# Optimization experiments

Measured on AMD Instinct MI355X. Metric: run time of the kernel, lower is better.

Reference implementation:

```python
import jax, jax.numpy as jnp
import numpy as np

R = 16
ALPHA = 16.0
SCALING = ALPHA / R  # = 1.0


def setup_inputs() -> dict:
    key = jax.random.key(0)
    k1, k2, k3 = jax.random.split(key, 3)
    x = jax.random.normal(k1, (4, 4096, 4096), dtype=jnp.float32)
    A = jax.random.normal(k2, (4096, R), dtype=jnp.float32)
    B = jax.random.normal(k3, (R, 4096), dtype=jnp.float32)
    return {"x": x, "A": A, "B": B}


def reference(x, A, B):
    # Faithful to torch: W_delta = A @ B * scaling; out = x @ W_delta
    # (dropout_p=0.0 so dropout is a no-op)
    W_delta = (A @ B) * SCALING  # [in, out]
    return jnp.matmul(x, W_delta)  # [b, s, out]
```

## Files before the change

kernel.cpp:

```cpp
#include <hip/hip_runtime.h>

constexpr int RANK = 16;
constexpr int K = 4096;
constexpr int N = 4096;
constexpr int M = 4 * 4096;
constexpr int KC = 512;
constexpr int NCHUNK = K / KC;

__global__ __launch_bounds__(256) void lora_fused(const float* __restrict__ x,
                                                  const float* __restrict__ A,
                                                  const float* __restrict__ B,
                                                  float* __restrict__ out) {
  const int lane = threadIdx.x & 63;
  const int tid = threadIdx.x;
  const int wave = tid >> 6;
  const int rbase = blockIdx.x * 16;
  const int r0 = rbase + wave * 4;

  __shared__ float4 As[KC * 4];
  __shared__ float Ts[16][RANK];

  const float4* __restrict__ A4 = reinterpret_cast<const float4*>(A);

  float vals[64];
#pragma unroll
  for (int i = 0; i < 64; ++i) vals[i] = 0.0f;

  for (int c = 0; c < NCHUNK; ++c) {
    __syncthreads();
#pragma unroll
    for (int q = 0; q < 8; ++q) {
      const int n = q * 256 + tid;
      const int k = n >> 2;
      const int s = n & 3;
      const int p = s ^ ((k >> 2) & 3);
      As[k * 4 + p] = A4[(size_t)c * 2048 + n];
    }
    __syncthreads();

    const int m = (lane >> 2) & 3;
#pragma unroll
    for (int kbi = 0; kbi < 8; ++kbi) {
      const int kl = kbi * 64 + lane;
      const size_t kg = (size_t)c * KC + kl;

      float xv[4];
#pragma unroll
      for (int r = 0; r < 4; ++r) xv[r] = x[(size_t)(r0 + r) * K + kg];

      float4 a[4];
#pragma unroll
      for (int s = 0; s < 4; ++s) a[s] = As[kl * 4 + (s ^ m)];

#pragma unroll
      for (int r = 0; r < 4; ++r) {
#pragma unroll
        for (int s = 0; s < 4; ++s) {
          vals[r * 16 + 4 * s + 0] = fmaf(xv[r], a[s].x, vals[r * 16 + 4 * s + 0]);
          vals[r * 16 + 4 * s + 1] = fmaf(xv[r], a[s].y, vals[r * 16 + 4 * s + 1]);
          vals[r * 16 + 4 * s + 2] = fmaf(xv[r], a[s].z, vals[r * 16 + 4 * s + 2]);
          vals[r * 16 + 4 * s + 3] = fmaf(xv[r], a[s].w, vals[r * 16 + 4 * s + 3]);
        }
      }
    }
  }

#define RSTEP(HALF)                                            \
  {                                                            \
    const bool hi = (lane & (HALF)) != 0;                      \
    _Pragma("unroll")                                          \
    for (int i = 0; i < (HALF); ++i) {                         \
      const float send = hi ? vals[i] : vals[i + (HALF)];      \
      const float keep = hi ? vals[i + (HALF)] : vals[i];      \
      vals[i] = keep + __shfl_xor(send, (HALF), 64);           \
    }                                                          \
  }
  RSTEP(32)
  RSTEP(16)
  RSTEP(8)
  RSTEP(4)
  RSTEP(2)
  RSTEP(1)
#undef RSTEP

  Ts[wave * 4 + (lane >> 4)][lane & 15] = vals[0];
  __syncthreads();

  const int n0 = wave * 1024 + lane * 4;
  const float4* __restrict__ B4 = reinterpret_cast<const float4*>(B);
  float4* __restrict__ out4 = reinterpret_cast<float4*>(out);

#pragma unroll 1
  for (int cc = 0; cc < 4; ++cc) {
    const int col = wave * 1024 + cc * 256 + lane * 4;

    float4 b[16];
#pragma unroll
    for (int j = 0; j < RANK; ++j) b[j] = B4[((size_t)j * N + col) >> 2];

#pragma unroll 1
    for (int r = 0; r < 16; ++r) {
      const float4* __restrict__ tr4 =
          reinterpret_cast<const float4*>(&Ts[r][0]);
      const float4 t0 = tr4[0];
      const float4 t1 = tr4[1];
      const float4 t2 = tr4[2];
      const float4 t3 = tr4[3];

      float4 acc;
      acc.x = acc.y = acc.z = acc.w = 0.0f;
      const float tsv[16] = {t0.x, t0.y, t0.z, t0.w, t1.x, t1.y, t1.z, t1.w,
                             t2.x, t2.y, t2.z, t2.w, t3.x, t3.y, t3.z, t3.w};
#pragma unroll
      for (int j = 0; j < RANK; ++j) {
        acc.x = fmaf(tsv[j], b[j].x, acc.x);
        acc.y = fmaf(tsv[j], b[j].y, acc.y);
        acc.z = fmaf(tsv[j], b[j].z, acc.z);
        acc.w = fmaf(tsv[j], b[j].w, acc.w);
      }
      out4[((size_t)(rbase + r) * N + col) >> 2] = acc;
    }
  }
  (void)n0;
}

extern "C" void kernel_launch(void* const* d_in, const int* in_sizes, int n_in,
                              void* d_out, int out_size, void* d_ws, size_t ws_size,
                              hipStream_t stream) {
  const float* x = (const float*)d_in[0];
  const float* A = (const float*)d_in[1];
  const float* B = (const float*)d_in[2];
  float* out = (float*)d_out;
  (void)d_ws; (void)ws_size;

  lora_fused<<<M / 16, 256, 0, stream>>>(x, A, B, out);
}
```

Baseline: 129.7 us.

## Double-buffer A chunks in LDS using direct global-to-LDS async loads

Replaces the register-staged copy of A into shared memory with __builtin_amdgcn_global_load_lds into a two-slot LDS buffer, prefetching the next chunk while the current one is consumed. The chunk size is halved to 256 so two buffers fit, and one barrier per chunk is removed. The goal is to hide A load latency and cut VGPR traffic. In exchange there are twice as many chunk iterations and barriers, and it depends on the swizzled global gather matching the LDS read pattern, with no explicit wait on the async loads before the barrier.

```diff
diff --git a/kernel.cpp b/kernel.cpp
--- a/kernel.cpp
+++ b/kernel.cpp
@@ -4,8 +4,11 @@
 constexpr int K = 4096;
 constexpr int N = 4096;
 constexpr int M = 4 * 4096;
-constexpr int KC = 512;
+constexpr int KC = 256;
 constexpr int NCHUNK = K / KC;
+
+typedef const __attribute__((address_space(1))) void gv_t;
+typedef __attribute__((address_space(3))) void lds_t;
 
 __global__ __launch_bounds__(256) void lora_fused(const float* __restrict__ x,
                                                   const float* __restrict__ A,
@@ -16,31 +19,41 @@
   const int wave = tid >> 6;
   const int rbase = blockIdx.x * 16;
   const int r0 = rbase + wave * 4;
+  const int m = (lane >> 2) & 3;
 
-  __shared__ float4 As[KC * 4];
+  __shared__ float4 As[2][KC * 4];
   __shared__ float Ts[16][RANK];
 
   const float4* __restrict__ A4 = reinterpret_cast<const float4*>(A);
+
+#define STAGE(b, cc)                                                        \
+  {                                                                         \
+    _Pragma("unroll")                                                       \
+    for (int q = 0; q < 4; ++q) {                                           \
+      const int nbase = q * 256 + wave * 64;                                \
+      const int n = nbase + lane;                                           \
+      const int g = (n & ~3) | ((n & 3) ^ ((n >> 4) & 3));                  \
+      __builtin_amdgcn_global_load_lds(                                     \
+          (gv_t*)(A4 + (size_t)(cc) * (KC * 4) + g),                        \
+          (lds_t*)&As[b][nbase], 16, 0, 0);                                 \
+    }                                                                       \
+  }
 
   float vals[64];
 #pragma unroll
   for (int i = 0; i < 64; ++i) vals[i] = 0.0f;
 
+  STAGE(0, 0)
+  __syncthreads();
+
   for (int c = 0; c < NCHUNK; ++c) {
-    __syncthreads();
+    const int cur = c & 1;
+    if (c + 1 < NCHUNK) STAGE(cur ^ 1, c + 1)
+
+    const float4* __restrict__ buf = As[cur];
+
 #pragma unroll
-    for (int q = 0; q < 8; ++q) {
-      const int n = q * 256 + tid;
-      const int k = n >> 2;
-      const int s = n & 3;
-      const int p = s ^ ((k >> 2) & 3);
-      As[k * 4 + p] = A4[(size_t)c * 2048 + n];
-    }
-    __syncthreads();
-
-    const int m = (lane >> 2) & 3;
-#pragma unroll
-    for (int kbi = 0; kbi < 8; ++kbi) {
+    for (int kbi = 0; kbi < KC / 64; ++kbi) {
       const int kl = kbi * 64 + lane;
       const size_t kg = (size_t)c * KC + kl;
 
@@ -50,7 +63,7 @@
 
       float4 a[4];
 #pragma unroll
-      for (int s = 0; s < 4; ++s) a[s] = As[kl * 4 + (s ^ m)];
+      for (int s = 0; s < 4; ++s) a[s] = buf[kl * 4 + (s ^ m)];
 
 #pragma unroll
       for (int r = 0; r < 4; ++r) {
@@ -63,7 +76,9 @@
         }
       }
     }
+    __syncthreads();
   }
+#undef STAGE
 
 #define RSTEP(HALF)                                            \
   {                                                            \
@@ -86,7 +101,6 @@
   Ts[wave * 4 + (lane >> 4)][lane & 15] = vals[0];
   __syncthreads();
 
-  const int n0 = wave * 1024 + lane * 4;
   const float4* __restrict__ B4 = reinterpret_cast<const float4*>(B);
   float4* __restrict__ out4 = reinterpret_cast<float4*>(out);
 
@@ -121,7 +135,6 @@
       out4[((size_t)(rbase + r) * N + col) >> 2] = acc;
     }
   }
-  (void)n0;
 }
 
 extern "C" void kernel_launch(void* const* d_in, const int* in_sizes, int n_in,
```

Measured after the change: 132.5 us. 2.2% more time.

## Split rank columns across two wave groups with 512-thread blocks

Applied to the files above, without the earlier changes.

Doubles the block size to 512 threads and splits the 16 rank accumulators between two wave groups, so each thread keeps 32 accumulators instead of 64. The shuffle reduction and the writes into Ts are adjusted to match, and the output phase now uses float2 stores spread over 8 waves. The goal is lower register pressure and higher occupancy to hide latency on the x stream. In exchange, each x element is now loaded twice, once per wave group, which raises global or L2 read traffic.

```diff
diff --git a/kernel.cpp b/kernel.cpp
--- a/kernel.cpp
+++ b/kernel.cpp
@@ -1,4 +1,5 @@
 #include <hip/hip_runtime.h>
+
 
 constexpr int RANK = 16;
 constexpr int K = 4096;
@@ -7,30 +8,33 @@
 constexpr int KC = 512;
 constexpr int NCHUNK = K / KC;
 
-__global__ __launch_bounds__(256) void lora_fused(const float* __restrict__ x,
-                                                  const float* __restrict__ A,
-                                                  const float* __restrict__ B,
-                                                  float* __restrict__ out) {
-  const int lane = threadIdx.x & 63;
+__global__ __launch_bounds__(512, 6) void lora_fused(const float* __restrict__ x,
+                                                     const float* __restrict__ A,
+                                                     const float* __restrict__ B,
+                                                     float* __restrict__ out) {
   const int tid = threadIdx.x;
-  const int wave = tid >> 6;
+  const int lane = tid & 63;
+  const int w = tid >> 6;
+  const int rg = w & 3;
+  const int jg = w >> 2;
   const int rbase = blockIdx.x * 16;
-  const int r0 = rbase + wave * 4;
+  const int r0 = rbase + rg * 4;
+  const int m = (lane >> 2) & 3;
 
   __shared__ float4 As[KC * 4];
   __shared__ float Ts[16][RANK];
 
   const float4* __restrict__ A4 = reinterpret_cast<const float4*>(A);
 
-  float vals[64];
+  float vals[32];
 #pragma unroll
-  for (int i = 0; i < 64; ++i) vals[i] = 0.0f;
+  for (int i = 0; i < 32; ++i) vals[i] = 0.0f;
 
   for (int c = 0; c < NCHUNK; ++c) {
     __syncthreads();
 #pragma unroll
-    for (int q = 0; q < 8; ++q) {
-      const int n = q * 256 + tid;
+    for (int q = 0; q < 4; ++q) {
+      const int n = q * 512 + tid;
       const int k = n >> 2;
       const int s = n & 3;
       const int p = s ^ ((k >> 2) & 3);
@@ -38,7 +42,6 @@
     }
     __syncthreads();
 
-    const int m = (lane >> 2) & 3;
 #pragma unroll
     for (int kbi = 0; kbi < 8; ++kbi) {
       const int kl = kbi * 64 + lane;
@@ -48,55 +51,58 @@
 #pragma unroll
       for (int r = 0; r < 4; ++r) xv[r] = x[(size_t)(r0 + r) * K + kg];
 
-      float4 a[4];
+      float4 a[2];
 #pragma unroll
-      for (int s = 0; s < 4; ++s) a[s] = As[kl * 4 + (s ^ m)];
+      for (int ss = 0; ss < 2; ++ss)
+        a[ss] = As[kl * 4 + ((2 * jg + ss) ^ m)];
 
 #pragma unroll
       for (int r = 0; r < 4; ++r) {
 #pragma unroll
-        for (int s = 0; s < 4; ++s) {
-          vals[r * 16 + 4 * s + 0] = fmaf(xv[r], a[s].x, vals[r * 16 + 4 * s + 0]);
-          vals[r * 16 + 4 * s + 1] = fmaf(xv[r], a[s].y, vals[r * 16 + 4 * s + 1]);
-          vals[r * 16 + 4 * s + 2] = fmaf(xv[r], a[s].z, vals[r * 16 + 4 * s + 2]);
-          vals[r * 16 + 4 * s + 3] = fmaf(xv[r], a[s].w, vals[r * 16 + 4 * s + 3]);
+        for (int ss = 0; ss < 2; ++ss) {
+          vals[r * 8 + ss * 4 + 0] = fmaf(xv[r], a[ss].x, vals[r * 8 + ss * 4 + 0]);
+          vals[r * 8 + ss * 4 + 1] = fmaf(xv[r], a[ss].y, vals[r * 8 + ss * 4 + 1]);
+          vals[r * 8 + ss * 4 + 2] = fmaf(xv[r], a[ss].z, vals[r * 8 + ss * 4 + 2]);
+          vals[r * 8 + ss * 4 + 3] = fmaf(xv[r], a[ss].w, vals[r * 8 + ss * 4 + 3]);
         }
       }
     }
   }
 
-#define RSTEP(HALF)                                            \
+#define FOLD(AH, LB)                                           \
   {                                                            \
-    const bool hi = (lane & (HALF)) != 0;                      \
+    const bool hi = (lane & (LB)) != 0;                        \
     _Pragma("unroll")                                          \
-    for (int i = 0; i < (HALF); ++i) {                         \
-      const float send = hi ? vals[i] : vals[i + (HALF)];      \
-      const float keep = hi ? vals[i + (HALF)] : vals[i];      \
-      vals[i] = keep + __shfl_xor(send, (HALF), 64);           \
+    for (int i = 0; i < (AH); ++i) {                           \
+      const float send = hi ? vals[i] : vals[i + (AH)];        \
+      const float keep = hi ? vals[i + (AH)] : vals[i];        \
+      vals[i] = keep + __shfl_xor(send, (LB), 64);             \
     }                                                          \
   }
-  RSTEP(32)
-  RSTEP(16)
-  RSTEP(8)
-  RSTEP(4)
-  RSTEP(2)
-  RSTEP(1)
-#undef RSTEP
+  FOLD(16, 32)
+  FOLD(8, 16)
+  FOLD(4, 8)
+  FOLD(2, 4)
+  FOLD(1, 2)
+#undef FOLD
+  vals[0] += __shfl_xor(vals[0], 1, 64);
 
-  Ts[wave * 4 + (lane >> 4)][lane & 15] = vals[0];
+  if (!(lane & 1)) {
+    const int e = lane >> 1;
+    Ts[rg * 4 + (e >> 3)][jg * 8 + (e & 7)] = vals[0];
+  }
   __syncthreads();
 
-  const int n0 = wave * 1024 + lane * 4;
-  const float4* __restrict__ B4 = reinterpret_cast<const float4*>(B);
-  float4* __restrict__ out4 = reinterpret_cast<float4*>(out);
+  const float2* __restrict__ B2 = reinterpret_cast<const float2*>(B);
+  float2* __restrict__ out2 = reinterpret_cast<float2*>(out);
 
 #pragma unroll 1
   for (int cc = 0; cc < 4; ++cc) {
-    const int col = wave * 1024 + cc * 256 + lane * 4;
+    const int col = w * 512 + cc * 128 + lane * 2;
 
-    float4 b[16];
+    float2 b[16];
 #pragma unroll
-    for (int j = 0; j < RANK; ++j) b[j] = B4[((size_t)j * N + col) >> 2];
+    for (int j = 0; j < RANK; ++j) b[j] = B2[((size_t)j * N + col) >> 1];
 
 #pragma unroll 1
     for (int r = 0; r < 16; ++r) {
@@ -106,22 +112,19 @@
       const float4 t1 = tr4[1];
       const float4 t2 = tr4[2];
       const float4 t3 = tr4[3];
-
-      float4 acc;
-      acc.x = acc.y = acc.z = acc.w = 0.0f;
       const float tsv[16] = {t0.x, t0.y, t0.z, t0.w, t1.x, t1.y, t1.z, t1.w,
                              t2.x, t2.y, t2.z, t2.w, t3.x, t3.y, t3.z, t3.w};
+
+      float2 acc;
+      acc.x = acc.y = 0.0f;
 #pragma unroll
       for (int j = 0; j < RANK; ++j) {
         acc.x = fmaf(tsv[j], b[j].x, acc.x);
         acc.y = fmaf(tsv[j], b[j].y, acc.y);
-        acc.z = fmaf(tsv[j], b[j].z, acc.z);
-        acc.w = fmaf(tsv[j], b[j].w, acc.w);
       }
-      out4[((size_t)(rbase + r) * N + col) >> 2] = acc;
+      out2[((size_t)(rbase + r) * N + col) >> 1] = acc;
     }
   }
-  (void)n0;
 }
 
 extern "C" void kernel_launch(void* const* d_in, const int* in_sizes, int n_in,
@@ -133,5 +136,5 @@
   float* out = (float*)d_out;
   (void)d_ws; (void)ws_size;
 
-  lora_fused<<<M / 16, 256, 0, stream>>>(x, A, B, out);
+  lora_fused<<<M / 16, 512, 0, stream>>>(x, A, B, out);
 }
```

Result: slower. 212.2 us (+63.7%).
